# Kernel tuning notes

Measured on AMD Instinct MI355X. Metric: run time of the kernel, lower is better.

## Reference

```python
import jax, jax.numpy as jnp
import numpy as np

B, H, W = 2, 224, 224
E, NH, DH, DFF = 64, 4, 16, 2048


def _conv2d(x, w, b):
    # stride-1 3x3 conv, padding=1 == SAME
    y = jax.lax.conv_general_dilated(x, w, (1, 1), 'SAME',
                                     dimension_numbers=('NCHW', 'OIHW', 'NCHW'))
    return y + b[None, :, None, None]


def _layer_norm(x, g, b, eps=1e-5):
    mu = x.mean(-1, keepdims=True)
    xc = x - mu
    var = (xc * xc).mean(-1, keepdims=True)
    return g * xc * jax.lax.rsqrt(var + eps) + b


def setup_inputs() -> dict:
    key = jax.random.key(0)
    ks = jax.random.split(key, 16)
    rn = lambda k, shape, s=0.05: jax.random.normal(k, shape, dtype=jnp.float32) * s
    z = lambda n: jnp.zeros((n,), jnp.float32)
    return {
        'x': jax.random.normal(ks[0], (B, 3, H, W), dtype=jnp.float32),
        'enc_w1': rn(ks[1], (64, 3, 3, 3)), 'enc_b1': z(64),
        'enc_w2': rn(ks[2], (64, 64, 3, 3)), 'enc_b2': z(64),
        'in_proj_w': rn(ks[3], (3 * E, E)), 'in_proj_b': z(3 * E),
        'out_proj_w': rn(ks[4], (E, E)), 'out_proj_b': z(E),
        'ln1_g': jnp.ones((E,), jnp.float32), 'ln1_b': z(E),
        'ffn_w1': rn(ks[5], (DFF, E)), 'ffn_b1': z(DFF),
        'ffn_w2': rn(ks[6], (E, DFF)), 'ffn_b2': z(E),
        'ln2_g': jnp.ones((E,), jnp.float32), 'ln2_b': z(E),
        'sf_w1': rn(ks[7], (32, 64, 3, 3)), 'sf_b1': z(32),
        'sf_w2': rn(ks[8], (9, 32, 3, 3)), 'sf_b2': z(9),
        'dec_w1': rn(ks[9], (64, 1, 3, 3)), 'dec_b1': z(64),
        'dec_w2': rn(ks[10], (1, 64, 3, 3)), 'dec_b2': z(1),
    }


def _forward(x, enc_w1, enc_b1, enc_w2, enc_b2,
             in_proj_w, in_proj_b, out_proj_w, out_proj_b,
             ln1_g, ln1_b, ffn_w1, ffn_b1, ffn_w2, ffn_b2, ln2_g, ln2_b,
             sf_w1, sf_b1, sf_w2, sf_b2, dec_w1, dec_b1, dec_w2, dec_b2):
    # ---- encoder ----
    e = jax.nn.relu(_conv2d(x, enc_w1, enc_b1))
    e = jax.nn.relu(_conv2d(e, enc_w2, enc_b2))
    b, c, h, w = e.shape
    # torch TransformerEncoderLayer default batch_first=False: [B, HW, E] is (S=B, N=HW, E)
    t = e.reshape(b, c, h * w).transpose(0, 2, 1)  # [S=B, N=HW, E]
    qkv = t @ in_proj_w.T + in_proj_b
    q, k, v = jnp.split(qkv, 3, axis=-1)
    S, N = q.shape[0], q.shape[1]
    q = q.reshape(S, N, NH, DH)
    k = k.reshape(S, N, NH, DH)
    v = v.reshape(S, N, NH, DH)
    scores = jnp.einsum('snhd,tnhd->nhst', q, k) / np.float32(np.sqrt(DH))
    attn = jnp.einsum('nhst,tnhd->snhd', jax.nn.softmax(scores, axis=-1), v)
    attn = attn.reshape(S, N, E) @ out_proj_w.T + out_proj_b
    t = _layer_norm(t + attn, ln1_g, ln1_b)
    ff = jax.nn.relu(t @ ffn_w1.T + ffn_b1) @ ffn_w2.T + ffn_b2
    t = _layer_norm(t + ff, ln2_g, ln2_b)
    enc2 = t.transpose(0, 2, 1).reshape(b, c, h, w)
    # ---- spatially adaptive per-pixel 3x3 filter (KPN-style) ----
    f = _conv2d(_conv2d(enc2, sf_w1, sf_b1), sf_w2, sf_b2)
    filters = f.reshape(b, 3, 3, h, w)  # per-pixel 3x3 kernel
    s = x.sum(axis=1)  # accumulate over the 3 input channels -> [B,H,W]
    sp = jnp.pad(s, ((0, 0), (1, 1), (1, 1)))
    patches = jnp.stack([sp[:, u:u + h, v:v + w] for u in range(3) for v in range(3)],
                        axis=1).reshape(b, 3, 3, h, w)
    fused = (filters * patches).sum(axis=(1, 2))[:, None]  # [B,1,H,W]
    # ---- decoder ----
    d = jax.nn.relu(_conv2d(fused, dec_w1, dec_b1))
    return jax.nn.sigmoid(_conv2d(d, dec_w2, dec_b2))


def reference(x, enc_w1, enc_b1, enc_w2, enc_b2,
              in_proj_w, in_proj_b, out_proj_w, out_proj_b,
              ln1_g, ln1_b, ffn_w1, ffn_b1, ffn_w2, ffn_b2, ln2_g, ln2_b,
              sf_w1, sf_b1, sf_w2, sf_b2, dec_w1, dec_b1, dec_w2, dec_b2):
    return _forward(x, enc_w1, enc_b1, enc_w2, enc_b2,
                    in_proj_w, in_proj_b, out_proj_w, out_proj_b,
                    ln1_g, ln1_b, ffn_w1, ffn_b1, ffn_w2, ffn_b2, ln2_g, ln2_b,
                    sf_w1, sf_b1, sf_w2, sf_b2, dec_w1, dec_b1, dec_w2, dec_b2)
```

## Files before the change

### kernel.cpp

```cpp
#include <hip/hip_runtime.h>
#include <hip/hip_bf16.h>
#include <cstddef>

#define HW   50176
#define NPIX 100352
#define IW   224

typedef unsigned short ushort_t;
typedef __attribute__((ext_vector_type(8))) short bf16x8;
typedef __attribute__((ext_vector_type(8))) unsigned short ushort8;
typedef __attribute__((ext_vector_type(4))) float f32x4;
typedef __attribute__((ext_vector_type(2))) _Float16 f16x2;
typedef __attribute__((ext_vector_type(8))) _Float16 f16x8;

__device__ inline ushort_t f2bf(float f) {
    __hip_bfloat16 h = __float2bfloat16(f);
    return __builtin_bit_cast(ushort_t, h);
}
__device__ inline float bf2f(ushort_t u) {
    return __uint_as_float(((unsigned)u) << 16);
}
__device__ inline bf16x8 ldg8(const ushort_t* p) {
    return *reinterpret_cast<const bf16x8*>(p);
}
__device__ inline void b2f8(const ushort_t* p, float* f) {
    ushort8 v = *reinterpret_cast<const ushort8*>(p);
#pragma unroll
    for (int i = 0; i < 8; i++) f[i] = bf2f(v[i]);
}
__device__ inline f16x2 pk16(float a, float b) {
    return __builtin_bit_cast(f16x2, __builtin_amdgcn_cvt_pkrtz(a, b));
}

__device__ inline void dma16(const ushort_t* g, ushort_t* l) {
    __builtin_amdgcn_global_load_lds(
        (const __attribute__((address_space(1))) void*)g,
        (__attribute__((address_space(3))) void*)l, 16, 0, 0);
}

__device__ void conv1_body(int gid, const float* __restrict__ x,
                           const float* __restrict__ w,
                           const float* __restrict__ bias,
                           ushort_t* __restrict__ out)
{
    int b = gid >= HW;
    int p = gid - b * HW;
    int y = p / IW, xx = p - y * IW;

    float v[27];
#pragma unroll
    for (int ci = 0; ci < 3; ci++) {
        const float* ip = x + ((size_t)(b * 3 + ci)) * HW;
#pragma unroll
        for (int t = 0; t < 9; t++) {
            int dy = t / 3 - 1, dx = t % 3 - 1;
            int yy = y + dy, xc = xx + dx;
            float tv = 0.f;
            if ((unsigned)yy < (unsigned)IW && (unsigned)xc < (unsigned)IW)
                tv = ip[yy * IW + xc];
            v[ci * 9 + t] = tv;
        }
    }
#pragma unroll
    for (int g = 0; g < 8; g++) {
        ushort8 o8;
#pragma unroll
        for (int i = 0; i < 8; i++) {
            int co = g * 8 + i;
            float a = bias[co];
            const float* wp = w + co * 27;
#pragma unroll
            for (int k = 0; k < 27; k++) a = fmaf(v[k], wp[k], a);
            o8[i] = f2bf(fmaxf(a, 0.f));
        }
        *reinterpret_cast<ushort8*>(out + (size_t)gid * 64 + g * 8) = o8;
    }
}

__global__ __launch_bounds__(256) void prep_conv1_k(
    const float* __restrict__ x,     const float* __restrict__ enc_w1,
    const float* __restrict__ enc_b1, ushort_t* __restrict__ E1b,
    const float* __restrict__ in_w,  ushort_t* __restrict__ in_wb,
    const float* __restrict__ out_w, ushort_t* __restrict__ out_wb,
    const float* __restrict__ w1,    ushort_t* __restrict__ w1p,
    const float* __restrict__ w2,    _Float16* __restrict__ w2s,
    const float* __restrict__ ec2,   ushort_t* __restrict__ wc2p,
    const float* __restrict__ s1,    ushort_t* __restrict__ ws1p,
    const float* __restrict__ s2,    ushort_t* __restrict__ ws2)
{
    if (blockIdx.x < 392) {
        conv1_body(blockIdx.x * 256 + threadIdx.x, x, enc_w1, enc_b1, E1b);
        return;
    }
    int idx = (blockIdx.x - 392) * 256 + threadIdx.x;
    if (idx < 12288) { in_wb[idx] = f2bf(in_w[idx]); return; }
    idx -= 12288;
    if (idx < 4096)  { out_wb[idx] = f2bf(out_w[idx]); return; }
    idx -= 4096;
    if (idx < 131072){
        int j = idx >> 6, e = idx & 63;
        int c = j >> 6, jl = j & 63;
        w1p[(size_t)c * 6144 + jl * 72 + e] = f2bf(w1[idx]);
        return;
    }
    idx -= 131072;
    if (idx < 131072){
        int j    = idx & 7;
        int lane = (idx >> 3) & 63;
        int rest = idx >> 9;
        int nt   = rest & 3;
        int cp   = rest >> 2;
        int p    = cp & 1;
        int c    = cp >> 1;
        int quad = lane >> 4;
        int e2   = nt * 16 + (lane & 15);
        int hl   = (j < 4) ? (quad * 4 + j) : (16 + quad * 4 + (j - 4));
        int hidden = c * 64 + p * 32 + hl;
        w2s[idx] = (_Float16)w2[(size_t)e2 * 2048 + hidden];
        return;
    }
    idx -= 131072;
    if (idx < 36864) {
        int j    = idx & 7;
        int lane = (idx >> 3) & 63;
        int rest = idx >> 9;
        int ks   = rest & 1;
        int nt   = (rest >> 1) & 3;
        int t    = rest >> 3;
        int co   = nt * 16 + (lane & 15);
        int ci   = ks * 32 + (lane >> 4) * 8 + j;
        wc2p[idx] = f2bf(ec2[((size_t)co * 64 + ci) * 9 + t]);
        return;
    }
    idx -= 36864;
    if (idx < 18432) {
        int j    = idx & 7;
        int lane = (idx >> 3) & 63;
        int rest = idx >> 9;
        int ks   = rest & 1;
        int nt   = (rest >> 1) & 1;
        int t    = rest >> 2;
        int co   = nt * 16 + (lane & 15);
        int ci   = ks * 32 + (lane >> 4) * 8 + j;
        ws1p[idx] = f2bf(s1[((size_t)co * 64 + ci) * 9 + t]);
        return;
    }
    idx -= 18432;
    if (idx < 4608)  {
        int ci = idx % 32;
        int t  = (idx / 32) % 9;
        int co = idx / 288;
        ws2[idx] = (co < 9) ? f2bf(s2[((size_t)co * 32 + ci) * 9 + t]) : (ushort_t)0;
        return;
    }
}

__global__ __launch_bounds__(256, 2) void enc2xf_k(
    const ushort_t* __restrict__ E1b, const ushort_t* __restrict__ Wc2p,
    const float* __restrict__ enc_b2,
    const ushort_t* __restrict__ Wqkv, const float* __restrict__ Bqkv,
    const ushort_t* __restrict__ Wo, const float* __restrict__ Bo,
    const float* __restrict__ g, const float* __restrict__ be,
    ushort_t* __restrict__ T1b)
{
    __shared__ ushort_t Q[128 * 200];
    __shared__ ushort_t WT[9216];

    int tid = threadIdx.x, wave = tid >> 6, lane = tid & 63;
    int lm = lane & 15, quad = lane >> 4;
    int p0 = blockIdx.x * 64;

    {
        int lr0 = wave * 32;
        int m[2], py[2], px[2];
#pragma unroll
        for (int mt = 0; mt < 2; mt++) {
            int lr = lr0 + mt * 16 + lm;
            int gp = p0 + (lr & 63);
            m[mt] = (lr >> 6) * HW + gp;
            py[mt] = gp / IW;
            px[mt] = gp - py[mt] * IW;
        }

        f32x4 acc[2][4] = {};
        bf16x8 zz = {};
        bf16x8 af[9][2][2];

#pragma unroll
        for (int t = 0; t < 9; t++) {
            int dy = t / 3 - 1, dx = t % 3 - 1;
#pragma unroll
            for (int mt = 0; mt < 2; mt++) {
                bool ok = (unsigned)(py[mt] + dy) < (unsigned)IW &&
                          (unsigned)(px[mt] + dx) < (unsigned)IW;
                const ushort_t* ip = E1b + (size_t)(m[mt] + dy * IW + dx) * 64 + quad * 8;
#pragma unroll
                for (int ks = 0; ks < 2; ks++)
                    af[t][mt][ks] = ok ? ldg8(ip + ks * 32) : zz;
            }
        }

#pragma unroll
        for (int t = 0; t < 9; t++) {
#pragma unroll
            for (int nt = 0; nt < 4; nt++)
#pragma unroll
                for (int ks = 0; ks < 2; ks++) {
                    bf16x8 bfv = ldg8(Wc2p + (size_t)(t * 8 + nt * 2 + ks) * 512 + lane * 8);
#pragma unroll
                    for (int mt = 0; mt < 2; mt++)
                        acc[mt][nt] = __builtin_amdgcn_mfma_f32_16x16x32_bf16(
                            af[t][mt][ks], bfv, acc[mt][nt], 0, 0, 0);
                }
        }

#pragma unroll
        for (int nt = 0; nt < 4; nt++) {
            float bv = enc_b2[nt * 16 + lm];
#pragma unroll
            for (int mt = 0; mt < 2; mt++)
#pragma unroll
                for (int r = 0; r < 4; r++) {
                    int lr = lr0 + mt * 16 + quad * 4 + r;
                    WT[lr * 72 + nt * 16 + lm] =
                        f2bf(fmaxf(acc[mt][nt][r] + bv, 0.f));
                }
        }
    }

    bf16x8 wq[12][2];
#pragma unroll
    for (int nt = 0; nt < 12; nt++)
#pragma unroll
        for (int ks = 0; ks < 2; ks++)
            wq[nt][ks] = ldg8(Wqkv + (size_t)(nt * 16 + lm) * 64 + ks * 32 + quad * 8);

    __syncthreads();

#pragma unroll
    for (int mt = 0; mt < 2; mt++) {
        int lA = mt * 64 + wave * 16;
        bf16x8 a[2];
#pragma unroll
        for (int ks = 0; ks < 2; ks++)
            a[ks] = *reinterpret_cast<const bf16x8*>(
                &WT[(lA + lm) * 72 + ks * 32 + quad * 8]);
        f32x4 acc[12] = {};
#pragma unroll
        for (int nt = 0; nt < 12; nt++)
#pragma unroll
            for (int ks = 0; ks < 2; ks++)
                acc[nt] = __builtin_amdgcn_mfma_f32_16x16x32_bf16(
                    a[ks], wq[nt][ks], acc[nt], 0, 0, 0);
        int lrow = lA + quad * 4;
#pragma unroll
        for (int nt = 0; nt < 12; nt++) {
            float bb = Bqkv[nt * 16 + lm];
#pragma unroll
            for (int r = 0; r < 4; r++)
                Q[(lrow + r) * 200 + nt * 16 + lm] = f2bf(acc[nt][r] + bb);
        }
    }
    __syncthreads();

    {
        int px = tid >> 2, h = tid & 3;
        ushort_t* r0 = &Q[px * 200 + h * 16];
        ushort_t* r1 = &Q[(64 + px) * 200 + h * 16];

        float q0[16], k0[16], v0[16], q1[16], k1[16], v1[16];
        b2f8(r0,       q0); b2f8(r0 + 8,   q0 + 8);
        b2f8(r0 + 64,  k0); b2f8(r0 + 72,  k0 + 8);
        b2f8(r0 + 128, v0); b2f8(r0 + 136, v0 + 8);
        b2f8(r1,       q1); b2f8(r1 + 8,   q1 + 8);
        b2f8(r1 + 64,  k1); b2f8(r1 + 72,  k1 + 8);
        b2f8(r1 + 128, v1); b2f8(r1 + 136, v1 + 8);

        float s00 = 0, s01 = 0, s10 = 0, s11 = 0;
#pragma unroll
        for (int d = 0; d < 16; d++) {
            s00 += q0[d] * k0[d]; s01 += q0[d] * k1[d];
            s10 += q1[d] * k0[d]; s11 += q1[d] * k1[d];
        }
        s00 *= 0.25f; s01 *= 0.25f; s10 *= 0.25f; s11 *= 0.25f;

        float m0 = fmaxf(s00, s01);
        float e00 = __expf(s00 - m0), e01 = __expf(s01 - m0);
        float i0 = 1.f / (e00 + e01);
        float p00 = e00 * i0, p01 = e01 * i0;

        float m1 = fmaxf(s10, s11);
        float e10 = __expf(s10 - m1), e11 = __expf(s11 - m1);
        float i1 = 1.f / (e10 + e11);
        float p10 = e10 * i1, p11 = e11 * i1;

#pragma unroll
        for (int c = 0; c < 2; c++) {
            ushort8 a0v, a1v;
#pragma unroll
            for (int i = 0; i < 8; i++) {
                int d = c * 8 + i;
                a0v[i] = f2bf(p00 * v0[d] + p01 * v1[d]);
                a1v[i] = f2bf(p10 * v0[d] + p11 * v1[d]);
            }
            *reinterpret_cast<ushort8*>(r0 + c * 8) = a0v;
            *reinterpret_cast<ushort8*>(r1 + c * 8) = a1v;
        }
    }

    bf16x8 wo[4][2];
#pragma unroll
    for (int nt = 0; nt < 4; nt++)
#pragma unroll
        for (int ks = 0; ks < 2; ks++)
            wo[nt][ks] = ldg8(Wo + (size_t)(nt * 16 + lm) * 64 + ks * 32 + quad * 8);

    __syncthreads();

#pragma unroll
    for (int mt = 0; mt < 2; mt++) {
        int lA = mt * 64 + wave * 16;
        size_t gbase = (size_t)((mt == 0 ? p0 : HW + p0) + wave * 16);
        bf16x8 a[2];
#pragma unroll
        for (int ks = 0; ks < 2; ks++)
            a[ks] = *reinterpret_cast<const bf16x8*>(
                &Q[(lA + lm) * 200 + ks * 32 + quad * 8]);
        f32x4 acc[4] = {};
#pragma unroll
        for (int nt = 0; nt < 4; nt++)
#pragma unroll
            for (int ks = 0; ks < 2; ks++)
                acc[nt] = __builtin_amdgcn_mfma_f32_16x16x32_bf16(
                    a[ks], wo[nt][ks], acc[nt], 0, 0, 0);

        float bv[4], gv[4], bev[4];
#pragma unroll
        for (int nt = 0; nt < 4; nt++) {
            bv[nt]  = Bo[nt * 16 + lm];
            gv[nt]  = g[nt * 16 + lm];
            bev[nt] = be[nt * 16 + lm];
        }
#pragma unroll
        for (int r = 0; r < 4; r++) {
            int lr = lA + quad * 4 + r;
            size_t row = gbase + quad * 4 + r;
            float v[4]; float s = 0.f;
#pragma unroll
            for (int nt = 0; nt < 4; nt++) {
                v[nt] = acc[nt][r] + bv[nt] + bf2f(WT[lr * 72 + nt * 16 + lm]);
                s += v[nt];
            }
#pragma unroll
            for (int o = 8; o; o >>= 1) s += __shfl_xor(s, o, 64);
            float mu = s * 0.015625f;
            float q = 0.f;
#pragma unroll
            for (int nt = 0; nt < 4; nt++) { v[nt] -= mu; q += v[nt] * v[nt]; }
#pragma unroll
            for (int o = 8; o; o >>= 1) q += __shfl_xor(q, o, 64);
            float rstd = rsqrtf(q * 0.015625f + 1e-5f);
#pragma unroll
            for (int nt = 0; nt < 4; nt++)
                T1b[row * 64 + nt * 16 + lm] = f2bf(gv[nt] * v[nt] * rstd + bev[nt]);
        }
    }
}

__global__ __launch_bounds__(256, 2) void neconv2_k(
    const ushort_t* __restrict__ In, const ushort_t* __restrict__ Wp,
    const float* __restrict__ bias, ushort_t* __restrict__ Ob)
{
    int tid = threadIdx.x, wave = tid >> 6, lane = tid & 63;
    int lm = lane & 15, quad = lane >> 4;
    int m0 = blockIdx.x * 128 + wave * 32;

    int m[2], py[2], px[2];
#pragma unroll
    for (int mt = 0; mt < 2; mt++) {
        int mm = m0 + mt * 16 + lm;
        m[mt] = mm;
        int p = mm - (mm >= HW ? HW : 0);
        py[mt] = p / IW;
        px[mt] = p - py[mt] * IW;
    }

    f32x4 acc[2][2] = {};
    bf16x8 zz = {};
    bf16x8 af[9][2][2];

#pragma unroll
    for (int t = 0; t < 9; t++) {
        int dy = t / 3 - 1, dx = t % 3 - 1;
#pragma unroll
        for (int mt = 0; mt < 2; mt++) {
            bool ok = (unsigned)(py[mt] + dy) < (unsigned)IW &&
                      (unsigned)(px[mt] + dx) < (unsigned)IW;
            const ushort_t* ip = In + (size_t)(m[mt] + dy * IW + dx) * 64 + quad * 8;
#pragma unroll
            for (int ks = 0; ks < 2; ks++)
                af[t][mt][ks] = ok ? ldg8(ip + ks * 32) : zz;
        }
    }

#pragma unroll
    for (int t = 0; t < 9; t++) {
#pragma unroll
        for (int nt = 0; nt < 2; nt++)
#pragma unroll
            for (int ks = 0; ks < 2; ks++) {
                bf16x8 bfv = ldg8(Wp + (size_t)(t * 4 + nt * 2 + ks) * 512 + lane * 8);
#pragma unroll
                for (int mt = 0; mt < 2; mt++)
                    acc[mt][nt] = __builtin_amdgcn_mfma_f32_16x16x32_bf16(
                        af[t][mt][ks], bfv, acc[mt][nt], 0, 0, 0);
            }
    }

#pragma unroll
    for (int nt = 0; nt < 2; nt++) {
        int col = nt * 16 + lm;
        float bv = bias[col];
#pragma unroll
        for (int mt = 0; mt < 2; mt++)
#pragma unroll
            for (int r = 0; r < 4; r++) {
                int row = m0 + mt * 16 + quad * 4 + r;
                Ob[(size_t)row * 32 + col] = f2bf(acc[mt][nt][r] + bv);
            }
    }
}

__global__ __launch_bounds__(512) void ffn9_k(
    const ushort_t* __restrict__ T1b,
    const ushort_t* __restrict__ W1p, const float* __restrict__ B1,
    const _Float16* __restrict__ W2s, const float* __restrict__ B2,
    const float* __restrict__ g, const float* __restrict__ be,
    ushort_t* __restrict__ OutTb)
{
    __shared__ ushort_t W1lds[3][6144];
    __shared__ ushort_t W2lds[3][4096];
    __shared__ float    B1l[2048];

    int tid = threadIdx.x, wave = tid >> 6, lane = tid & 63;
    int lm = lane & 15, quad = lane >> 4;
    int rowbase = blockIdx.x * 256 + wave * 32;

    *reinterpret_cast<float4*>(&B1l[tid * 4]) =
        *reinterpret_cast<const float4*>(B1 + tid * 4);

    bf16x8 Bt[2][2];
#pragma unroll
    for (int mt = 0; mt < 2; mt++)
#pragma unroll
        for (int ks = 0; ks < 2; ks++)
            Bt[mt][ks] = ldg8(T1b + (size_t)(rowbase + mt * 16 + lm) * 64 + ks * 32 + quad * 8);

    __syncthreads();

    auto dma_chunk = [&](int c, int pb) {
        const ushort_t* g1 = W1p + (size_t)c * 6144;
        const ushort_t* g2 = (const ushort_t*)(W2s + (size_t)c * 4096);
#pragma unroll
        for (int i = 0; i < 3; i++) {
            int idx = i * 8 + wave;
            if (idx < 12)
                dma16(g1 + idx * 512 + lane * 8, &W1lds[pb][idx * 512]);
            else if (idx < 20)
                dma16(g2 + (idx - 12) * 512 + lane * 8,
                      &W2lds[pb][(idx - 12) * 512]);
        }
    };

    dma_chunk(0, 0);
    dma_chunk(1, 1);

    f32x4 acc[2][4] = {};

    for (int c = 0; c < 32; c++) {
        int pb = c % 3;

        if (c < 31) {
            if (wave < 4) asm volatile("s_waitcnt vmcnt(3)" ::: "memory");
            else          asm volatile("s_waitcnt vmcnt(2)" ::: "memory");
        } else {
            asm volatile("s_waitcnt vmcnt(0)" ::: "memory");
        }
        __builtin_amdgcn_s_barrier();
        asm volatile("" ::: "memory");

        if (c + 2 < 32) dma_chunk(c + 2, (c + 2) % 3);

        const ushort_t* w1l = &W1lds[pb][0];
        const ushort_t* w2l = &W2lds[pb][0];

#pragma unroll
        for (int p = 0; p < 2; p++) {
            bf16x8 w1r[2][2];
            f16x8  w2r[4];
            float4 b1r[2];
#pragma unroll
            for (int s = 0; s < 2; s++) {
                int ul = p * 2 + s;
#pragma unroll
                for (int ks = 0; ks < 2; ks++)
                    w1r[s][ks] = *reinterpret_cast<const bf16x8*>(
                        &w1l[(ul * 16 + lm) * 72 + ks * 32 + quad * 8]);
                b1r[s] = *reinterpret_cast<const float4*>(
                    &B1l[(c * 4 + ul) * 16 + quad * 4]);
            }
#pragma unroll
            for (int nt = 0; nt < 4; nt++)
                w2r[nt] = *reinterpret_cast<const f16x8*>(
                    &w2l[((p * 4 + nt) * 64 + lane) * 8]);

            f32x4 h[2][2];
#pragma unroll
            for (int s = 0; s < 2; s++) {
                f32x4 binit = {b1r[s].x, b1r[s].y, b1r[s].z, b1r[s].w};
#pragma unroll
                for (int mt = 0; mt < 2; mt++) h[s][mt] = binit;
            }

            __builtin_amdgcn_s_setprio(1);
#pragma unroll
            for (int s = 0; s < 2; s++)
#pragma unroll
                for (int ks = 0; ks < 2; ks++)
#pragma unroll
                    for (int mt = 0; mt < 2; mt++)
                        h[s][mt] = __builtin_amdgcn_mfma_f32_16x16x32_bf16(
                            w1r[s][ks], Bt[mt][ks], h[s][mt], 0, 0, 0);

            f16x8 aH[2];
#pragma unroll
            for (int mt = 0; mt < 2; mt++) {
                f16x2 t0 = pk16(fmaxf(h[0][mt][0], 0.f), fmaxf(h[0][mt][1], 0.f));
                f16x2 t1 = pk16(fmaxf(h[0][mt][2], 0.f), fmaxf(h[0][mt][3], 0.f));
                f16x2 t2 = pk16(fmaxf(h[1][mt][0], 0.f), fmaxf(h[1][mt][1], 0.f));
                f16x2 t3 = pk16(fmaxf(h[1][mt][2], 0.f), fmaxf(h[1][mt][3], 0.f));
                f16x8 a;
                a[0] = t0[0]; a[1] = t0[1]; a[2] = t1[0]; a[3] = t1[1];
                a[4] = t2[0]; a[5] = t2[1]; a[6] = t3[0]; a[7] = t3[1];
                aH[mt] = a;
            }

#pragma unroll
            for (int nt = 0; nt < 4; nt++)
#pragma unroll
                for (int mt = 0; mt < 2; mt++)
                    acc[mt][nt] = __builtin_amdgcn_mfma_f32_16x16x32_f16(
                        aH[mt], w2r[nt], acc[mt][nt], 0, 0, 0);
            __builtin_amdgcn_s_setprio(0);
        }
    }

    float b2v[4], gv[4], bev[4];
#pragma unroll
    for (int nt = 0; nt < 4; nt++) {
        b2v[nt] = B2[nt * 16 + lm];
        gv[nt]  = g[nt * 16 + lm];
        bev[nt] = be[nt * 16 + lm];
    }
#pragma unroll
    for (int mt = 0; mt < 2; mt++)
#pragma unroll
        for (int r = 0; r < 4; r++) {
            int row = rowbase + mt * 16 + quad * 4 + r;
            float v[4]; float s = 0.f;
#pragma unroll
            for (int nt = 0; nt < 4; nt++) {
                v[nt] = acc[mt][nt][r] + b2v[nt] +
                        bf2f(T1b[(size_t)row * 64 + nt * 16 + lm]);
                s += v[nt];
            }
#pragma unroll
            for (int o = 8; o; o >>= 1) s += __shfl_xor(s, o, 64);
            float mu = s * 0.015625f;
            float q = 0.f;
#pragma unroll
            for (int nt = 0; nt < 4; nt++) { v[nt] -= mu; q += v[nt] * v[nt]; }
#pragma unroll
            for (int o = 8; o; o >>= 1) q += __shfl_xor(q, o, 64);
            float rstd = rsqrtf(q * 0.015625f + 1e-5f);
#pragma unroll
            for (int nt = 0; nt < 4; nt++)
                OutTb[(size_t)row * 64 + nt * 16 + lm] =
                    f2bf(gv[nt] * v[nt] * rstd + bev[nt]);
        }
}

__global__ __launch_bounds__(256) void sf2kpn_k(
    const ushort_t* __restrict__ In,
    const ushort_t* __restrict__ Wsw,
    const float* __restrict__ bias,
    const float* __restrict__ x,
    float* __restrict__ fused)
{
    __shared__ float Fl[128 * 12];
    int tid = threadIdx.x, wave = tid >> 6, lane = tid & 63;
    int lm = lane & 15, quad = lane >> 4;
    int m0 = blockIdx.x * 128 + wave * 32;

    int m[2], py[2], px[2];
#pragma unroll
    for (int mt = 0; mt < 2; mt++) {
        int mm = m0 + mt * 16 + lm;
        m[mt] = mm;
        int p = mm - (mm >= HW ? HW : 0);
        py[mt] = p / IW;
        px[mt] = p - py[mt] * IW;
    }

    f32x4 acc[2] = {};
    bf16x8 zz = {};
    bf16x8 af[9][2];
    bf16x8 wv[9];

#pragma unroll
    for (int t = 0; t < 9; t++) {
        int dy = t / 3 - 1, dx = t % 3 - 1;
#pragma unroll
        for (int mt = 0; mt < 2; mt++) {
            bool ok = (unsigned)(py[mt] + dy) < (unsigned)IW &&
                      (unsigned)(px[mt] + dx) < (unsigned)IW;
            af[t][mt] = ok ? ldg8(In + (size_t)(m[mt] + dy * IW + dx) * 32 + quad * 8) : zz;
        }
    }
#pragma unroll
    for (int t = 0; t < 9; t++)
        wv[t] = ldg8(Wsw + ((size_t)lm * 9 + t) * 32 + quad * 8);

#pragma unroll
    for (int t = 0; t < 9; t++)
#pragma unroll
        for (int mt = 0; mt < 2; mt++)
            acc[mt] = __builtin_amdgcn_mfma_f32_16x16x32_bf16(af[t][mt], wv[t], acc[mt], 0, 0, 0);

    if (lm < 9) {
        float bv = bias[lm];
#pragma unroll
        for (int mt = 0; mt < 2; mt++)
#pragma unroll
            for (int r = 0; r < 4; r++) {
                int lrow = wave * 32 + mt * 16 + quad * 4 + r;
                Fl[lrow * 12 + lm] = acc[mt][r] + bv;
            }
    }
    __syncthreads();

    if (tid < 128) {
        int gid = blockIdx.x * 128 + tid;
        int b = gid >= HW;
        int p = gid - b * HW;
        int y = p / IW, xx = p - y * IW;
        const float* fp = &Fl[tid * 12];
        const float* xp = x + (size_t)b * 3 * HW;
        float a = 0.f;
#pragma unroll
        for (int u = 0; u < 3; u++) {
            int yy = y + u - 1;
            if ((unsigned)yy >= (unsigned)IW) continue;
#pragma unroll
            for (int v = 0; v < 3; v++) {
                int xc = xx + v - 1;
                if ((unsigned)xc >= (unsigned)IW) continue;
                int o = yy * IW + xc;
                float s = xp[o] + xp[HW + o] + xp[2 * HW + o];
                a += fp[u * 3 + v] * s;
            }
        }
        fused[gid] = a;
    }
}

__global__ __launch_bounds__(256) void dec1_k(
    const float* __restrict__ fused,
    const float* __restrict__ w1, const float* __restrict__ b1,
    _Float16* __restrict__ Hb)
{
    int gid = blockIdx.x * 256 + threadIdx.x;
    int b = gid >= HW;
    int p = gid - b * HW;
    int y = p / IW, xx = p - y * IW;
    const float* ip = fused + (size_t)b * HW;

    float F[9];
#pragma unroll
    for (int s = 0; s < 9; s++) {
        int yy = y + s / 3 - 1, xc = xx + s % 3 - 1;
        float t = 0.f;
        if ((unsigned)yy < (unsigned)IW && (unsigned)xc < (unsigned)IW)
            t = ip[yy * IW + xc];
        F[s] = t;
    }
    _Float16* op = Hb + (size_t)gid * 64;
#pragma unroll
    for (int g = 0; g < 8; g++) {
        f16x8 o;
#pragma unroll
        for (int i = 0; i < 8; i++) {
            int c = g * 8 + i;
            float h = b1[c];
            const float* wp = w1 + c * 9;
#pragma unroll
            for (int s = 0; s < 9; s++) h = fmaf(F[s], wp[s], h);
            o[i] = (_Float16)fmaxf(h, 0.f);
        }
        *reinterpret_cast<f16x8*>(op + g * 8) = o;
    }
}

__global__ __launch_bounds__(256) void dec2_k(
    const _Float16* __restrict__ Hb,
    const float* __restrict__ w2, const float* __restrict__ b2,
    float* __restrict__ out)
{
    int gid = blockIdx.x * 256 + threadIdx.x;
    int b = gid >= HW;
    int p = gid - b * HW;
    int y = p / IW, xx = p - y * IW;
    (void)b;

    float acc = b2[0];
#pragma unroll
    for (int n = 0; n < 9; n++) {
        int dy = n / 3 - 1, dx = n % 3 - 1;
        int yy = y + dy, xc = xx + dx;
        if ((unsigned)yy >= (unsigned)IW || (unsigned)xc >= (unsigned)IW) continue;
        const _Float16* hp = Hb + (size_t)(gid + dy * IW + dx) * 64;
#pragma unroll
        for (int g = 0; g < 8; g++) {
            f16x8 hv = *reinterpret_cast<const f16x8*>(hp + g * 8);
#pragma unroll
            for (int i = 0; i < 8; i++)
                acc = fmaf((float)hv[i], w2[(g * 8 + i) * 9 + n], acc);
        }
    }
    out[gid] = 1.f / (1.f + __expf(-acc));
}

extern "C" void kernel_launch(void* const* d_in, const int* in_sizes, int n_in,
                              void* d_out, int out_size, void* d_ws, size_t ws_size,
                              hipStream_t stream)
{
    const float* x      = (const float*)d_in[0];
    const float* enc_w1 = (const float*)d_in[1];
    const float* enc_b1 = (const float*)d_in[2];
    const float* enc_w2 = (const float*)d_in[3];
    const float* enc_b2 = (const float*)d_in[4];
    const float* in_w   = (const float*)d_in[5];
    const float* in_b   = (const float*)d_in[6];
    const float* out_w  = (const float*)d_in[7];
    const float* out_b  = (const float*)d_in[8];
    const float* ln1_g  = (const float*)d_in[9];
    const float* ln1_b  = (const float*)d_in[10];
    const float* ffn_w1 = (const float*)d_in[11];
    const float* ffn_b1 = (const float*)d_in[12];
    const float* ffn_w2 = (const float*)d_in[13];
    const float* ffn_b2 = (const float*)d_in[14];
    const float* ln2_g  = (const float*)d_in[15];
    const float* ln2_b  = (const float*)d_in[16];
    const float* sf_w1  = (const float*)d_in[17];
    const float* sf_b1  = (const float*)d_in[18];
    const float* sf_w2  = (const float*)d_in[19];
    const float* sf_b2  = (const float*)d_in[20];
    const float* dec_w1 = (const float*)d_in[21];
    const float* dec_b1 = (const float*)d_in[22];
    const float* dec_w2 = (const float*)d_in[23];
    const float* dec_b2 = (const float*)d_in[24];

    float* ws = (float*)d_ws;
    const size_t SZ = (size_t)NPIX * 64;

    ushort_t* E1b  = (ushort_t*)(ws + 5 * SZ);
    ushort_t* Tb   = (ushort_t*)(ws + 11 * SZ / 2);
    ushort_t* wu   = (ushort_t*)(ws + 6 * SZ);
    ushort_t* in_wb  = wu;
    ushort_t* out_wb = wu + 12288;
    ushort_t* w1p    = wu + 16384;
    _Float16* w2s    = (_Float16*)(wu + 212992);
    ushort_t* wc2p   = wu + 344064;
    ushort_t* ws1p   = wu + 385536;
    ushort_t* ws2    = wu + 408576;
    float*    base3 = ws + 3 * SZ;
    ushort_t* s1b   = (ushort_t*)base3;
    float*    fused = base3 + SZ / 2;
    _Float16* Hb    = (_Float16*)(ws + 4 * SZ);

    prep_conv1_k<<<1714, 256, 0, stream>>>(
        x, enc_w1, enc_b1, E1b,
        in_w, in_wb, out_w, out_wb, ffn_w1, w1p,
        ffn_w2, w2s, enc_w2, wc2p, sf_w1, ws1p, sf_w2, ws2);

    enc2xf_k<<<784, 256, 0, stream>>>(E1b, wc2p, enc_b2,
                                      in_wb, in_b, out_wb, out_b,
                                      ln1_g, ln1_b, Tb);
    ffn9_k<<<392, 512, 0, stream>>>(Tb, w1p, ffn_b1, w2s, ffn_b2, ln2_g, ln2_b, E1b);
    neconv2_k<<<784, 256, 0, stream>>>(E1b, ws1p, sf_b1, s1b);
    sf2kpn_k<<<784, 256, 0, stream>>>(s1b, ws2, sf_b2, x, fused);
    dec1_k<<<392, 256, 0, stream>>>(fused, dec_w1, dec_b1, Hb);
    dec2_k<<<392, 256, 0, stream>>>(Hb, dec_w2, dec_b2, (float*)d_out);
}
```

Measured before the change: 304.3 us.

## Split FFN hidden dimension across wave pairs with 64-row tiles and LDS reduction

The FFN kernel changes its work split. Each group of four waves now handles 64 rows instead of 32. The two wave halves each take half of every 64-wide hidden chunk, instead of one wave looping over both halves. Partial output accumulators are summed through LDS before the residual and layernorm epilogue. This gives each weight fragment read from LDS twice as much MFMA reuse, but doubles the accumulator register count and adds a final reduction and barrier. It also sets launch_bounds to 2 blocks per CU and packs the LDS buffers into one manually laid-out array.

```diff
diff --git a/kernel.cpp b/kernel.cpp
--- a/kernel.cpp
+++ b/kernel.cpp
@@ -431,27 +431,31 @@
     }
 }
 
-__global__ __launch_bounds__(512) void ffn9_k(
+__global__ __launch_bounds__(512, 2) void ffn13_k(
     const ushort_t* __restrict__ T1b,
     const ushort_t* __restrict__ W1p, const float* __restrict__ B1,
     const _Float16* __restrict__ W2s, const float* __restrict__ B2,
     const float* __restrict__ g, const float* __restrict__ be,
     ushort_t* __restrict__ OutTb)
 {
-    __shared__ ushort_t W1lds[3][6144];
-    __shared__ ushort_t W2lds[3][4096];
-    __shared__ float    B1l[2048];
+    __shared__ __align__(16) unsigned char SMEM[69632];
+    ushort_t* W1base = (ushort_t*)SMEM;
+    ushort_t* W2base = (ushort_t*)(SMEM + 36864);
+    float*    B1l    = (float*)(SMEM + 61440);
+    float*    red    = (float*)SMEM;
 
     int tid = threadIdx.x, wave = tid >> 6, lane = tid & 63;
     int lm = lane & 15, quad = lane >> 4;
-    int rowbase = blockIdx.x * 256 + wave * 32;
+    int pid = wave & 3;
+    int ph  = wave >> 2;
+    int rowbase = blockIdx.x * 256 + pid * 64;
 
     *reinterpret_cast<float4*>(&B1l[tid * 4]) =
         *reinterpret_cast<const float4*>(B1 + tid * 4);
 
-    bf16x8 Bt[2][2];
-#pragma unroll
-    for (int mt = 0; mt < 2; mt++)
+    bf16x8 Bt[4][2];
+#pragma unroll
+    for (int mt = 0; mt < 4; mt++)
 #pragma unroll
         for (int ks = 0; ks < 2; ks++)
             Bt[mt][ks] = ldg8(T1b + (size_t)(rowbase + mt * 16 + lm) * 64 + ks * 32 + quad * 8);
@@ -465,17 +469,17 @@
         for (int i = 0; i < 3; i++) {
             int idx = i * 8 + wave;
             if (idx < 12)
-                dma16(g1 + idx * 512 + lane * 8, &W1lds[pb][idx * 512]);
+                dma16(g1 + idx * 512 + lane * 8, W1base + pb * 6144 + idx * 512);
             else if (idx < 20)
                 dma16(g2 + (idx - 12) * 512 + lane * 8,
-                      &W2lds[pb][(idx - 12) * 512]);
+                      W2base + pb * 4096 + (idx - 12) * 512);
         }
     };
 
     dma_chunk(0, 0);
     dma_chunk(1, 1);
 
-    f32x4 acc[2][4] = {};
+    f32x4 acc[4][4] = {};
 
     for (int c = 0; c < 32; c++) {
         int pb = c % 3;
@@ -491,103 +495,121 @@
 
         if (c + 2 < 32) dma_chunk(c + 2, (c + 2) % 3);
 
-        const ushort_t* w1l = &W1lds[pb][0];
-        const ushort_t* w2l = &W2lds[pb][0];
-
-#pragma unroll
-        for (int p = 0; p < 2; p++) {
-            bf16x8 w1r[2][2];
-            f16x8  w2r[4];
-            float4 b1r[2];
-#pragma unroll
-            for (int s = 0; s < 2; s++) {
-                int ul = p * 2 + s;
-#pragma unroll
-                for (int ks = 0; ks < 2; ks++)
-                    w1r[s][ks] = *reinterpret_cast<const bf16x8*>(
-                        &w1l[(ul * 16 + lm) * 72 + ks * 32 + quad * 8]);
-                b1r[s] = *reinterpret_cast<const float4*>(
-                    &B1l[(c * 4 + ul) * 16 + quad * 4]);
+        const ushort_t* w1l = W1base + pb * 6144;
+        const ushort_t* w2l = W2base + pb * 4096;
+
+        bf16x8 w1r[2][2];
+        f16x8  w2r[4];
+        float4 b1r[2];
+#pragma unroll
+        for (int s = 0; s < 2; s++) {
+            int ul = ph * 2 + s;
+#pragma unroll
+            for (int ks = 0; ks < 2; ks++)
+                w1r[s][ks] = *reinterpret_cast<const bf16x8*>(
+                    &w1l[(ul * 16 + lm) * 72 + ks * 32 + quad * 8]);
+            b1r[s] = *reinterpret_cast<const float4*>(
+                &B1l[(c * 4 + ul) * 16 + quad * 4]);
+        }
+#pragma unroll
+        for (int nt = 0; nt < 4; nt++)
+            w2r[nt] = *reinterpret_cast<const f16x8*>(
+                &w2l[((ph * 4 + nt) * 64 + lane) * 8]);
+
+        f32x4 h[2][4];
+#pragma unroll
+        for (int s = 0; s < 2; s++) {
+            f32x4 binit = {b1r[s].x, b1r[s].y, b1r[s].z, b1r[s].w};
+#pragma unroll
+            for (int mt = 0; mt < 4; mt++) h[s][mt] = binit;
+        }
+
+        __builtin_amdgcn_s_setprio(1);
+#pragma unroll
+        for (int s = 0; s < 2; s++)
+#pragma unroll
+            for (int ks = 0; ks < 2; ks++)
+#pragma unroll
+                for (int mt = 0; mt < 4; mt++)
+                    h[s][mt] = __builtin_amdgcn_mfma_f32_16x16x32_bf16(
+                        w1r[s][ks], Bt[mt][ks], h[s][mt], 0, 0, 0);
+
+        f16x8 aH[4];
+#pragma unroll
+        for (int mt = 0; mt < 4; mt++) {
+            f16x2 t0 = pk16(fmaxf(h[0][mt][0], 0.f), fmaxf(h[0][mt][1], 0.f));
+            f16x2 t1 = pk16(fmaxf(h[0][mt][2], 0.f), fmaxf(h[0][mt][3], 0.f));
+            f16x2 t2 = pk16(fmaxf(h[1][mt][0], 0.f), fmaxf(h[1][mt][1], 0.f));
+            f16x2 t3 = pk16(fmaxf(h[1][mt][2], 0.f), fmaxf(h[1][mt][3], 0.f));
+            f16x8 a;
+            a[0] = t0[0]; a[1] = t0[1]; a[2] = t1[0]; a[3] = t1[1];
+            a[4] = t2[0]; a[5] = t2[1]; a[6] = t3[0]; a[7] = t3[1];
+            aH[mt] = a;
+        }
+
+#pragma unroll
+        for (int nt = 0; nt < 4; nt++)
+#pragma unroll
+            for (int mt = 0; mt < 4; mt++)
+                acc[mt][nt] = __builtin_amdgcn_mfma_f32_16x16x32_f16(
+                    aH[mt], w2r[nt], acc[mt][nt], 0, 0, 0);
+        __builtin_amdgcn_s_setprio(0);
+    }
+
+    __syncthreads();
+    if (wave >= 4) {
+        float* dst = red + pid * 4096;
+#pragma unroll
+        for (int mt = 0; mt < 4; mt++)
+#pragma unroll
+            for (int nt = 0; nt < 4; nt++)
+                *reinterpret_cast<f32x4*>(dst + (mt * 4 + nt) * 256 + lane * 4) =
+                    acc[mt][nt];
+    }
+    __syncthreads();
+    if (wave < 4) {
+        const float* src = red + pid * 4096;
+#pragma unroll
+        for (int mt = 0; mt < 4; mt++)
+#pragma unroll
+            for (int nt = 0; nt < 4; nt++)
+                acc[mt][nt] += *reinterpret_cast<const f32x4*>(
+                    src + (mt * 4 + nt) * 256 + lane * 4);
+
+        float b2v[4], gv[4], bev[4];
+#pragma unroll
+        for (int nt = 0; nt < 4; nt++) {
+            b2v[nt] = B2[nt * 16 + lm];
+            gv[nt]  = g[nt * 16 + lm];
+            bev[nt] = be[nt * 16 + lm];
+        }
+#pragma unroll
+        for (int mt = 0; mt < 4; mt++)
+#pragma unroll
+            for (int r = 0; r < 4; r++) {
+                int row = rowbase + mt * 16 + quad * 4 + r;
+                float v[4]; float s = 0.f;
+#pragma unroll
+                for (int nt = 0; nt < 4; nt++) {
+                    v[nt] = acc[mt][nt][r] + b2v[nt] +
+                            bf2f(T1b[(size_t)row * 64 + nt * 16 + lm]);
+                    s += v[nt];
+                }
+#pragma unroll
+                for (int o = 8; o; o >>= 1) s += __shfl_xor(s, o, 64);
+                float mu = s * 0.015625f;
+                float q = 0.f;
+#pragma unroll
+                for (int nt = 0; nt < 4; nt++) { v[nt] -= mu; q += v[nt] * v[nt]; }
+#pragma unroll
+                for (int o = 8; o; o >>= 1) q += __shfl_xor(q, o, 64);
+                float rstd = rsqrtf(q * 0.015625f + 1e-5f);
+#pragma unroll
+                for (int nt = 0; nt < 4; nt++)
+                    OutTb[(size_t)row * 64 + nt * 16 + lm] =
+                        f2bf(gv[nt] * v[nt] * rstd + bev[nt]);
             }
-#pragma unroll
-            for (int nt = 0; nt < 4; nt++)
-                w2r[nt] = *reinterpret_cast<const f16x8*>(
-                    &w2l[((p * 4 + nt) * 64 + lane) * 8]);
-
-            f32x4 h[2][2];
-#pragma unroll
-            for (int s = 0; s < 2; s++) {
-                f32x4 binit = {b1r[s].x, b1r[s].y, b1r[s].z, b1r[s].w};
-#pragma unroll
-                for (int mt = 0; mt < 2; mt++) h[s][mt] = binit;
-            }
-
-            __builtin_amdgcn_s_setprio(1);
-#pragma unroll
-            for (int s = 0; s < 2; s++)
-#pragma unroll
-                for (int ks = 0; ks < 2; ks++)
-#pragma unroll
-                    for (int mt = 0; mt < 2; mt++)
-                        h[s][mt] = __builtin_amdgcn_mfma_f32_16x16x32_bf16(
-                            w1r[s][ks], Bt[mt][ks], h[s][mt], 0, 0, 0);
-
-            f16x8 aH[2];
-#pragma unroll
-            for (int mt = 0; mt < 2; mt++) {
-                f16x2 t0 = pk16(fmaxf(h[0][mt][0], 0.f), fmaxf(h[0][mt][1], 0.f));
-                f16x2 t1 = pk16(fmaxf(h[0][mt][2], 0.f), fmaxf(h[0][mt][3], 0.f));
-                f16x2 t2 = pk16(fmaxf(h[1][mt][0], 0.f), fmaxf(h[1][mt][1], 0.f));
-                f16x2 t3 = pk16(fmaxf(h[1][mt][2], 0.f), fmaxf(h[1][mt][3], 0.f));
-                f16x8 a;
-                a[0] = t0[0]; a[1] = t0[1]; a[2] = t1[0]; a[3] = t1[1];
-                a[4] = t2[0]; a[5] = t2[1]; a[6] = t3[0]; a[7] = t3[1];
-                aH[mt] = a;
-            }
-
-#pragma unroll
-            for (int nt = 0; nt < 4; nt++)
-#pragma unroll
-                for (int mt = 0; mt < 2; mt++)
-                    acc[mt][nt] = __builtin_amdgcn_mfma_f32_16x16x32_f16(
-                        aH[mt], w2r[nt], acc[mt][nt], 0, 0, 0);
-            __builtin_amdgcn_s_setprio(0);
-        }
-    }
-
-    float b2v[4], gv[4], bev[4];
-#pragma unroll
-    for (int nt = 0; nt < 4; nt++) {
-        b2v[nt] = B2[nt * 16 + lm];
-        gv[nt]  = g[nt * 16 + lm];
-        bev[nt] = be[nt * 16 + lm];
-    }
-#pragma unroll
-    for (int mt = 0; mt < 2; mt++)
-#pragma unroll
-        for (int r = 0; r < 4; r++) {
-            int row = rowbase + mt * 16 + quad * 4 + r;
-            float v[4]; float s = 0.f;
-#pragma unroll
-            for (int nt = 0; nt < 4; nt++) {
-                v[nt] = acc[mt][nt][r] + b2v[nt] +
-                        bf2f(T1b[(size_t)row * 64 + nt * 16 + lm]);
-                s += v[nt];
-            }
-#pragma unroll
-            for (int o = 8; o; o >>= 1) s += __shfl_xor(s, o, 64);
-            float mu = s * 0.015625f;
-            float q = 0.f;
-#pragma unroll
-            for (int nt = 0; nt < 4; nt++) { v[nt] -= mu; q += v[nt] * v[nt]; }
-#pragma unroll
-            for (int o = 8; o; o >>= 1) q += __shfl_xor(q, o, 64);
-            float rstd = rsqrtf(q * 0.015625f + 1e-5f);
-#pragma unroll
-            for (int nt = 0; nt < 4; nt++)
-                OutTb[(size_t)row * 64 + nt * 16 + lm] =
-                    f2bf(gv[nt] * v[nt] * rstd + bev[nt]);
-        }
+    }
 }
 
 __global__ __launch_bounds__(256) void sf2kpn_k(
@@ -796,7 +818,7 @@
     enc2xf_k<<<784, 256, 0, stream>>>(E1b, wc2p, enc_b2,
                                       in_wb, in_b, out_wb, out_b,
                                       ln1_g, ln1_b, Tb);
-    ffn9_k<<<392, 512, 0, stream>>>(Tb, w1p, ffn_b1, w2s, ffn_b2, ln2_g, ln2_b, E1b);
+    ffn13_k<<<392, 512, 0, stream>>>(Tb, w1p, ffn_b1, w2s, ffn_b2, ln2_g, ln2_b, E1b);
     neconv2_k<<<784, 256, 0, stream>>>(E1b, ws1p, sf_b1, s1b);
     sf2kpn_k<<<784, 256, 0, stream>>>(s1b, ws2, sf_b2, x, fused);
     dec1_k<<<392, 256, 0, stream>>>(fused, dec_w1, dec_b1, Hb);
```

New measurement: 341.9 us. 12.4% more time.

## Fuse decoder convs into one tiled kernel with shared-memory intermediate

Applied to the files above, without the earlier changes.

Merges the two decoder conv kernels into a single kernel that processes 16x16 output tiles. Each block loads a 20x20 halo of the fused map, computes the 64-channel ReLU intermediate for an 18x18 halo into LDS, then evaluates the second 3x3 conv and sigmoid from LDS. This removes the round trip of the 64-channel fp16 intermediate through global memory and one launch, in exchange for recomputing halo pixels and using about 47KB of LDS per block, which may limit occupancy.

```diff
diff --git a/kernel.cpp b/kernel.cpp
--- a/kernel.cpp
+++ b/kernel.cpp
@@ -674,70 +674,84 @@
     }
 }
 
-__global__ __launch_bounds__(256) void dec1_k(
+__global__ __launch_bounds__(256) void dec_tile_k(
     const float* __restrict__ fused,
     const float* __restrict__ w1, const float* __restrict__ b1,
-    _Float16* __restrict__ Hb)
-{
-    int gid = blockIdx.x * 256 + threadIdx.x;
-    int b = gid >= HW;
-    int p = gid - b * HW;
-    int y = p / IW, xx = p - y * IW;
-    const float* ip = fused + (size_t)b * HW;
-
-    float F[9];
-#pragma unroll
-    for (int s = 0; s < 9; s++) {
-        int yy = y + s / 3 - 1, xc = xx + s % 3 - 1;
-        float t = 0.f;
-        if ((unsigned)yy < (unsigned)IW && (unsigned)xc < (unsigned)IW)
-            t = ip[yy * IW + xc];
-        F[s] = t;
-    }
-    _Float16* op = Hb + (size_t)gid * 64;
-#pragma unroll
-    for (int g = 0; g < 8; g++) {
-        f16x8 o;
-#pragma unroll
-        for (int i = 0; i < 8; i++) {
-            int c = g * 8 + i;
-            float h = b1[c];
-            const float* wp = w1 + c * 9;
-#pragma unroll
-            for (int s = 0; s < 9; s++) h = fmaf(F[s], wp[s], h);
-            o[i] = (_Float16)fmaxf(h, 0.f);
-        }
-        *reinterpret_cast<f16x8*>(op + g * 8) = o;
-    }
-}
-
-__global__ __launch_bounds__(256) void dec2_k(
-    const _Float16* __restrict__ Hb,
     const float* __restrict__ w2, const float* __restrict__ b2,
     float* __restrict__ out)
 {
-    int gid = blockIdx.x * 256 + threadIdx.x;
-    int b = gid >= HW;
-    int p = gid - b * HW;
-    int y = p / IW, xx = p - y * IW;
-    (void)b;
-
-    float acc = b2[0];
-#pragma unroll
-    for (int n = 0; n < 9; n++) {
-        int dy = n / 3 - 1, dx = n % 3 - 1;
-        int yy = y + dy, xc = xx + dx;
-        if ((unsigned)yy >= (unsigned)IW || (unsigned)xc >= (unsigned)IW) continue;
-        const _Float16* hp = Hb + (size_t)(gid + dy * IW + dx) * 64;
-#pragma unroll
-        for (int g = 0; g < 8; g++) {
-            f16x8 hv = *reinterpret_cast<const f16x8*>(hp + g * 8);
-#pragma unroll
-            for (int i = 0; i < 8; i++)
-                acc = fmaf((float)hv[i], w2[(g * 8 + i) * 9 + n], acc);
-        }
-    }
-    out[gid] = 1.f / (1.f + __expf(-acc));
+    __shared__ float    Fs[400];
+    __shared__ _Float16 Hl[324 * 72];
+
+    int tid = threadIdx.x;
+    int b   = blockIdx.x / 196;
+    int rem = blockIdx.x - b * 196;
+    int ty0 = (rem / 14) * 16;
+    int tx0 = (rem % 14) * 16;
+    const float* fp = fused + (size_t)b * HW;
+
+    for (int k = tid; k < 400; k += 256) {
+        int fy = k / 20, fx = k - fy * 20;
+        int gy = ty0 + fy - 2, gx = tx0 + fx - 2;
+        float t = 0.f;
+        if ((unsigned)gy < (unsigned)IW && (unsigned)gx < (unsigned)IW)
+            t = fp[gy * IW + gx];
+        Fs[k] = t;
+    }
+    __syncthreads();
+
+    for (int ph = tid; ph < 324; ph += 256) {
+        int hy = ph / 18, hx = ph - hy * 18;
+        int gy = ty0 + hy - 1, gx = tx0 + hx - 1;
+        _Float16* op = &Hl[ph * 72];
+        if ((unsigned)gy >= (unsigned)IW || (unsigned)gx >= (unsigned)IW) {
+            f16x8 z = {};
+#pragma unroll
+            for (int g = 0; g < 8; g++)
+                *reinterpret_cast<f16x8*>(op + g * 8) = z;
+        } else {
+            float F[9];
+#pragma unroll
+            for (int s = 0; s < 9; s++)
+                F[s] = Fs[(hy + s / 3) * 20 + (hx + s % 3)];
+#pragma unroll
+            for (int g = 0; g < 8; g++) {
+                f16x8 o;
+#pragma unroll
+                for (int i = 0; i < 8; i++) {
+                    int c = g * 8 + i;
+                    float h = b1[c];
+                    const float* wp = w1 + c * 9;
+#pragma unroll
+                    for (int s = 0; s < 9; s++) h = fmaf(F[s], wp[s], h);
+                    o[i] = (_Float16)fmaxf(h, 0.f);
+                }
+                *reinterpret_cast<f16x8*>(op + g * 8) = o;
+            }
+        }
+    }
+    __syncthreads();
+
+    {
+        int ty = tid >> 4, tx = tid & 15;
+        int gy = ty0 + ty, gx = tx0 + tx;
+        float acc = b2[0];
+#pragma unroll
+        for (int n = 0; n < 9; n++) {
+            int dy = n / 3 - 1, dx = n % 3 - 1;
+            int yy = gy + dy, xc = gx + dx;
+            if ((unsigned)yy >= (unsigned)IW || (unsigned)xc >= (unsigned)IW) continue;
+            const _Float16* hp = &Hl[((ty + 1 + dy) * 18 + (tx + 1 + dx)) * 72];
+#pragma unroll
+            for (int g = 0; g < 8; g++) {
+                f16x8 hv = *reinterpret_cast<const f16x8*>(hp + g * 8);
+#pragma unroll
+                for (int i = 0; i < 8; i++)
+                    acc = fmaf((float)hv[i], w2[(g * 8 + i) * 9 + n], acc);
+            }
+        }
+        out[(size_t)b * HW + gy * IW + gx] = 1.f / (1.f + __expf(-acc));
+    }
 }
 
 extern "C" void kernel_launch(void* const* d_in, const int* in_sizes, int n_in,
@@ -786,7 +800,6 @@
     float*    base3 = ws + 3 * SZ;
     ushort_t* s1b   = (ushort_t*)base3;
     float*    fused = base3 + SZ / 2;
-    _Float16* Hb    = (_Float16*)(ws + 4 * SZ);
 
     prep_conv1_k<<<1714, 256, 0, stream>>>(
         x, enc_w1, enc_b1, E1b,
@@ -799,6 +812,6 @@
     ffn9_k<<<392, 512, 0, stream>>>(Tb, w1p, ffn_b1, w2s, ffn_b2, ln2_g, ln2_b, E1b);
     neconv2_k<<<784, 256, 0, stream>>>(E1b, ws1p, sf_b1, s1b);
     sf2kpn_k<<<784, 256, 0, stream>>>(s1b, ws2, sf_b2, x, fused);
-    dec1_k<<<392, 256, 0, stream>>>(fused, dec_w1, dec_b1, Hb);
-    dec2_k<<<392, 256, 0, stream>>>(Hb, dec_w2, dec_b2, (float*)d_out);
-}
+    dec_tile_k<<<392, 256, 0, stream>>>(fused, dec_w1, dec_b1, dec_w2, dec_b2,
+                                        (float*)d_out);
+}
```

After: 297.2 us (median of 2 runs). -2.3%, faster.
